# Optimization experiments

Hardware: AMD Instinct MI355X
Metric: run time of the kernel (lower is better)

The kernel has to match this reference:

```python
import jax, jax.numpy as jnp
import numpy as np


def _sparsify24(w):
    """2:4 structured sparsity: per contiguous group of 4 along the last dim,
    keep the 2 largest-magnitude entries, zero the other 2 (soft_threshold24)."""
    m, n = w.shape
    g = w.reshape(m, n // 4, 4)
    a = jnp.abs(g)
    # 2nd-largest magnitude in each group = index 2 of ascending sort of 4
    thresh = jnp.sort(a, axis=-1)[..., 2:3]
    mask = a >= thresh
    return (g * mask).reshape(m, n)


def setup_inputs() -> dict:
    key = jax.random.key(0)
    k1, k2, k3 = jax.random.split(key, 3)
    B, S, DIN, DOUT = 4, 4096, 1024, 1024
    x = jax.random.normal(k1, (B, S, DIN), dtype=jnp.float32)
    weight = jax.random.normal(k2, (DIN, DOUT), dtype=jnp.float32) * 0.02
    bias = jax.random.normal(k3, (DOUT,), dtype=jnp.float32) * 0.02
    sparse_scale = jnp.ones((1,), dtype=jnp.float32)
    return {"x": x, "weight": weight, "bias": bias, "sparse_scale": sparse_scale}


def reference(x, weight, bias, sparse_scale):
    # get_sparse_weight: cast weight to fp16, apply 2:4 sparsity, multiply by
    # learnable fp32 scale (promotes to fp32 as in torch half*float).
    w_sparse = _sparsify24(weight.astype(jnp.float16)).astype(jnp.float32) * sparse_scale
    # fake_fp8_mm: both operands cast to fp16, accumulate/output in fp32.
    a = x.reshape(-1, x.shape[-1]).astype(jnp.float16)          # [B*S, DIN]
    b = w_sparse.astype(jnp.float16)                             # [DIN, DOUT]
    out = jnp.matmul(a, b, preferred_element_type=jnp.float32)   # [B*S, DOUT] fp32
    out = out.reshape(*x.shape[:-1], -1) + bias
    return out
```

## Files before the change

### kernel.cpp

```cpp
#include <hip/hip_runtime.h>
#include <hip/hip_fp16.h>
#include <stdint.h>

#define M_TOT 16384
#define N_TOT 1024
#define K_TOT 1024

typedef _Float16 f16x8 __attribute__((ext_vector_type(8)));
typedef float f32x4 __attribute__((ext_vector_type(4)));
typedef unsigned short ushort4v __attribute__((ext_vector_type(4)));

__device__ inline void gl2lds16(const void* g, void* l) {
    __builtin_amdgcn_global_load_lds(
        (const __attribute__((address_space(1))) void*)(uintptr_t)(g),
        (__attribute__((address_space(3))) void*)(uint32_t)(uintptr_t)(l),
        16, 0, 0);
}

__global__ void __launch_bounds__(256) prep_and_cast(const float* __restrict__ X,
                                                     const float* __restrict__ W,
                                                     const float* __restrict__ scale_p,
                                                     _Float16* __restrict__ Xh,
                                                     _Float16* __restrict__ wT) {
    const int tid = threadIdx.x;
    if (blockIdx.x < 256) {
        __shared__ _Float16 sT[64 * 68 + 4];
        const float scale = scale_p[0];
        const int k0 = (blockIdx.x & 15) * 64;
        const int n0 = (blockIdx.x >> 4) * 64;
        const int r = tid >> 4;
        const int c4 = (tid & 15) * 4;
#pragma unroll
        for (int p = 0; p < 4; ++p) {
            const int k = p * 16 + r;
            float4 w4 = *(const float4*)&W[(size_t)(k0 + k) * N_TOT + n0 + c4];
            _Float16 h0 = (_Float16)w4.x, h1 = (_Float16)w4.y, h2 = (_Float16)w4.z, h3 = (_Float16)w4.w;
            float a0 = fabsf((float)h0), a1 = fabsf((float)h1), a2 = fabsf((float)h2), a3 = fabsf((float)h3);
            float lo01 = fminf(a0, a1), hi01 = fmaxf(a0, a1);
            float lo23 = fminf(a2, a3), hi23 = fmaxf(a2, a3);
            float s2 = fmaxf(fminf(hi01, hi23), fmaxf(lo01, lo23));
            sT[(c4 + 0) * 68 + k] = (_Float16)(((a0 >= s2) ? (float)h0 : 0.0f) * scale);
            sT[(c4 + 1) * 68 + k] = (_Float16)(((a1 >= s2) ? (float)h1 : 0.0f) * scale);
            sT[(c4 + 2) * 68 + k] = (_Float16)(((a2 >= s2) ? (float)h2 : 0.0f) * scale);
            sT[(c4 + 3) * 68 + k] = (_Float16)(((a3 >= s2) ? (float)h3 : 0.0f) * scale);
        }
        __syncthreads();
#pragma unroll
        for (int p = 0; p < 4; ++p) {
            const int n = p * 16 + r;
            ushort4v v = *(const ushort4v*)&sT[n * 68 + c4];
            *(ushort4v*)&wT[(size_t)(n0 + n) * K_TOT + k0 + c4] = v;
        }
    } else {
        size_t i = ((size_t)(blockIdx.x - 256) * 256 + tid) * 8;
        float4 x0 = *(const float4*)&X[i];
        float4 x1 = *(const float4*)&X[i + 4];
        f16x8 h;
        h[0] = (_Float16)x0.x; h[1] = (_Float16)x0.y; h[2] = (_Float16)x0.z; h[3] = (_Float16)x0.w;
        h[4] = (_Float16)x1.x; h[5] = (_Float16)x1.y; h[6] = (_Float16)x1.z; h[7] = (_Float16)x1.w;
        *(f16x8*)&Xh[i] = h;
    }
}

__global__ void __launch_bounds__(512) gemm_bt(const _Float16* __restrict__ A,
                                               const _Float16* __restrict__ Bt,
                                               const float* __restrict__ bias,
                                               float* __restrict__ C) {
    __shared__ _Float16 sA[2][256 * 32];
    __shared__ _Float16 sB[2][128 * 32];
    const int tid = threadIdx.x;
    const int id = blockIdx.x;
    const int by = id & 63;
    const int bx = id >> 6;
    const int wave = tid >> 6;
    const int lane = tid & 63;
    const int wm = wave >> 1;
    const int wn = wave & 1;
    const int quad = lane >> 4;
    const int l16 = lane & 15;

    const int srow = tid >> 2;
    const int scol = (tid & 3) * 8;

    const _Float16* gA = A + ((size_t)(by * 256 + srow)) * K_TOT + scol;
    const _Float16* gB = Bt + ((size_t)(bx * 128 + srow)) * K_TOT + scol;
    const int soff = srow * 32 + scol;

    f32x4 acc[4][4];
#pragma unroll
    for (int i = 0; i < 4; ++i)
#pragma unroll
        for (int j = 0; j < 4; ++j)
            acc[i][j] = (f32x4){0.f, 0.f, 0.f, 0.f};

    for (int k0 = 0; k0 < K_TOT; k0 += 64) {
        __syncthreads();
        gl2lds16(gA + k0,                            &sA[0][soff]);
        gl2lds16(gA + k0 + (size_t)128 * K_TOT,      &sA[0][soff + 128 * 32]);
        gl2lds16(gA + k0 + 32,                       &sA[1][soff]);
        gl2lds16(gA + k0 + 32 + (size_t)128 * K_TOT, &sA[1][soff + 128 * 32]);
        gl2lds16(gB + k0,                            &sB[0][soff]);
        gl2lds16(gB + k0 + 32,                       &sB[1][soff]);
        __syncthreads();

#pragma unroll
        for (int s = 0; s < 2; ++s) {
            f16x8 af[4], bf[4];
#pragma unroll
            for (int i = 0; i < 4; ++i) {
                af[i] = *(const f16x8*)&sA[s][(wm * 64 + i * 16 + l16) * 32 + quad * 8];
                bf[i] = *(const f16x8*)&sB[s][(wn * 64 + i * 16 + l16) * 32 + quad * 8];
            }
#pragma unroll
            for (int i = 0; i < 4; ++i)
#pragma unroll
                for (int j = 0; j < 4; ++j)
                    acc[i][j] = __builtin_amdgcn_mfma_f32_16x16x32_f16(af[i], bf[j], acc[i][j], 0, 0, 0);
        }
    }

#pragma unroll
    for (int j = 0; j < 4; ++j) {
        const int col = bx * 128 + wn * 64 + j * 16 + l16;
        const float bj = bias[col];
#pragma unroll
        for (int i = 0; i < 4; ++i) {
            const int row0 = by * 256 + wm * 64 + i * 16 + quad * 4;
#pragma unroll
            for (int r = 0; r < 4; ++r) {
                C[(size_t)(row0 + r) * N_TOT + col] = acc[i][j][r] + bj;
            }
        }
    }
}

extern "C" void kernel_launch(void* const* d_in, const int* in_sizes, int n_in,
                              void* d_out, int out_size, void* d_ws, size_t ws_size,
                              hipStream_t stream) {
    const float* x      = (const float*)d_in[0];
    const float* weight = (const float*)d_in[1];
    const float* bias   = (const float*)d_in[2];
    const float* sscale = (const float*)d_in[3];
    float* out = (float*)d_out;

    _Float16* wT = (_Float16*)d_ws;
    _Float16* xh = (_Float16*)((char*)d_ws + (size_t)2 * 1024 * 1024);

    prep_and_cast<<<256 + (M_TOT * K_TOT / 8) / 256, 256, 0, stream>>>(x, weight, sscale, xh, wT);
    gemm_bt<<<512, 512, 0, stream>>>(xh, wT, bias, out);
}
```

Measured before the change: 149.5 us.

## Double-buffer LDS tiles to overlap global loads with MFMA compute

```diff
diff --git a/kernel.cpp b/kernel.cpp
--- a/kernel.cpp
+++ b/kernel.cpp
@@ -66,8 +66,8 @@
                                                const _Float16* __restrict__ Bt,
                                                const float* __restrict__ bias,
                                                float* __restrict__ C) {
-    __shared__ _Float16 sA[2][256 * 32];
-    __shared__ _Float16 sB[2][128 * 32];
+    __shared__ _Float16 sA[2][2][256 * 32];
+    __shared__ _Float16 sB[2][2][128 * 32];
     const int tid = threadIdx.x;
     const int id = blockIdx.x;
     const int by = id & 63;
@@ -93,23 +93,35 @@
         for (int j = 0; j < 4; ++j)
             acc[i][j] = (f32x4){0.f, 0.f, 0.f, 0.f};
 
-    for (int k0 = 0; k0 < K_TOT; k0 += 64) {
+#define STAGE(p, b)                                                              \
+    do {                                                                         \
+        const int kk = (p) * 64;                                                 \
+        gl2lds16(gA + kk,                            &sA[b][0][soff]);           \
+        gl2lds16(gA + kk + (size_t)128 * K_TOT,      &sA[b][0][soff + 128 * 32]);\
+        gl2lds16(gA + kk + 32,                       &sA[b][1][soff]);           \
+        gl2lds16(gA + kk + 32 + (size_t)128 * K_TOT, &sA[b][1][soff + 128 * 32]);\
+        gl2lds16(gB + kk,                            &sB[b][0][soff]);           \
+        gl2lds16(gB + kk + 32,                       &sB[b][1][soff]);           \
+    } while (0)
+
+    STAGE(0, 0);
+
+#pragma unroll 2
+    for (int p = 0; p < 16; ++p) {
+        const int cur = p & 1;
+        const int nxt = cur ^ 1;
         __syncthreads();
-        gl2lds16(gA + k0,                            &sA[0][soff]);
-        gl2lds16(gA + k0 + (size_t)128 * K_TOT,      &sA[0][soff + 128 * 32]);
-        gl2lds16(gA + k0 + 32,                       &sA[1][soff]);
-        gl2lds16(gA + k0 + 32 + (size_t)128 * K_TOT, &sA[1][soff + 128 * 32]);
-        gl2lds16(gB + k0,                            &sB[0][soff]);
-        gl2lds16(gB + k0 + 32,                       &sB[1][soff]);
-        __syncthreads();
+
+        const int pn = (p + 1 < 16) ? (p + 1) : 0;
+        STAGE(pn, nxt);
 
 #pragma unroll
         for (int s = 0; s < 2; ++s) {
             f16x8 af[4], bf[4];
 #pragma unroll
             for (int i = 0; i < 4; ++i) {
-                af[i] = *(const f16x8*)&sA[s][(wm * 64 + i * 16 + l16) * 32 + quad * 8];
-                bf[i] = *(const f16x8*)&sB[s][(wn * 64 + i * 16 + l16) * 32 + quad * 8];
+                af[i] = *(const f16x8*)&sA[cur][s][(wm * 64 + i * 16 + l16) * 32 + quad * 8];
+                bf[i] = *(const f16x8*)&sB[cur][s][(wn * 64 + i * 16 + l16) * 32 + quad * 8];
             }
 #pragma unroll
             for (int i = 0; i < 4; ++i)
@@ -118,6 +130,7 @@
                     acc[i][j] = __builtin_amdgcn_mfma_f32_16x16x32_f16(af[i], bf[j], acc[i][j], 0, 0, 0);
         }
     }
+#undef STAGE
 
 #pragma unroll
     for (int j = 0; j < 4; ++j) {
```

After: 154.4 us. 1.03x slower.
